# Kernel tuning notes

Measured on AMD Instinct MI355X. Metric: run time of the kernel, lower is better.

## Reference

```python
import jax, jax.numpy as jnp
import numpy as np

B, S, H, NH = 16, 384, 1024, 16
HD = H // NH  # head_dim = 64

def setup_inputs() -> dict:
    key = jax.random.key(0)
    k1, k2, k3 = jax.random.split(key, 3)
    activation = jax.random.normal(k1, (B, S, H), dtype=jnp.float32)
    attention_mask = jnp.zeros((B, 1, 1, S), dtype=jnp.float32)  # additive mask
    qkv_weight = jax.random.normal(k2, (H, 3 * H), dtype=jnp.float32) * 0.02
    qkv_bias = jax.random.normal(k3, (3 * H,), dtype=jnp.float32) * 0.02
    return {"activation": activation, "attention_mask": attention_mask,
            "qkv_weight": qkv_weight, "qkv_bias": qkv_bias}

def reference(activation, attention_mask, qkv_weight, qkv_bias):
    # op1: fused QKV projection
    qkv = activation @ qkv_weight + qkv_bias            # [B,S,3H]
    q, k, v = jnp.split(qkv, 3, axis=-1)                # each [B,S,H]
    # op2-6: split heads -> [B,NH,S,HD]
    def heads(x):
        return x.reshape(B, S, NH, HD).transpose(0, 2, 1, 3)
    q, k, v = heads(q), heads(k), heads(v)
    # op7: QK^T
    scores = jnp.einsum('bhqd,bhkd->bhqk', q, k)        # [B,NH,S,S]
    # op8: scale + mask + softmax (scale applied to scores, then additive mask)
    scale = 1.0 / np.sqrt(HD).astype(np.float32)
    probs = jax.nn.softmax(scores * scale + attention_mask, axis=-1)
    # op9: weighted V
    out = jnp.einsum('bhqk,bhkd->bhqd', probs, v)       # [B,NH,S,HD]
    # op10: concat heads
    return out.transpose(0, 2, 1, 3).reshape(B, S, H)
```

## Files before the change

### kernel.cpp

```cpp
#include <hip/hip_runtime.h>
#include <hip/hip_bf16.h>

#define BB 16
#define SS 384
#define HH 1024
#define NH 16
#define HD 64
#define MM (BB*SS)
#define KK HH
#define N3 (3*HH)

typedef float f32x4 __attribute__((ext_vector_type(4)));
typedef __bf16 bf16x8 __attribute__((ext_vector_type(8)));
typedef unsigned short us8 __attribute__((ext_vector_type(8)));
typedef unsigned short us4 __attribute__((ext_vector_type(4)));
typedef unsigned int u32x4 __attribute__((ext_vector_type(4)));

__device__ __forceinline__ void gload_lds16(const void* g, void* l) {
    __builtin_amdgcn_global_load_lds(
        (const __attribute__((address_space(1))) void*)g,
        (__attribute__((address_space(3))) void*)l, 16, 0, 0);
}

__device__ __forceinline__ unsigned short f2b(float f) {
    __bf16 h = (__bf16)f;
    return __builtin_bit_cast(unsigned short, h);
}

__global__ __launch_bounds__(256) void cvt_x(const float4* __restrict__ in,
                                             us4* __restrict__ out, int n4) {
    int i = blockIdx.x * 256 + threadIdx.x;
    if (i < n4) {
        float4 v = in[i];
        us4 o;
        o.x = f2b(v.x); o.y = f2b(v.y); o.z = f2b(v.z); o.w = f2b(v.w);
        out[i] = o;
    }
}

__global__ __launch_bounds__(256) void cvt_w(const float* __restrict__ Wf,
                                             __bf16* __restrict__ WT) {
    __shared__ float tile[32][33];
    const int n0 = blockIdx.x * 32, k0 = blockIdx.y * 32;
    const int t = threadIdx.x;
    const int tj = t & 31, ti = t >> 5;
#pragma unroll
    for (int p = 0; p < 4; ++p) {
        int i = p * 8 + ti;
        tile[i][tj] = Wf[(size_t)(k0 + i) * N3 + n0 + tj];
    }
    __syncthreads();
#pragma unroll
    for (int p = 0; p < 4; ++p) {
        int jj = p * 8 + ti;
        WT[(size_t)(n0 + jj) * KK + k0 + tj] = (__bf16)tile[tj][jj];
    }
}

__global__ __launch_bounds__(256) void qkv_gemm(const __bf16* __restrict__ Xb,
                                                const __bf16* __restrict__ WT,
                                                const float* __restrict__ bias,
                                                __bf16* __restrict__ QKb,
                                                __bf16* __restrict__ VTg) {
    __shared__ __bf16 As[128 * 32];
    __shared__ __bf16 Bs[128 * 32];
    const int t = threadIdx.x;
    const int w = t >> 6, lane = t & 63;
    const int wr = w >> 1, wc = w & 1;
    const int l15 = lane & 15, lg = lane >> 4;
    const int m0 = blockIdx.y * 128, n0 = blockIdx.x * 128;

    f32x4 acc[4][4] = {};

    for (int k0 = 0; k0 < KK; k0 += 32) {
#pragma unroll
        for (int i = 0; i < 2; ++i) {
            int slab = w * 2 + i;
            int row = slab * 16 + (lane >> 2);
            int ck = lane & 3;
            gload_lds16(Xb + (size_t)(m0 + row) * KK + k0 + ck * 8, &As[slab * 512]);
            gload_lds16(WT + (size_t)(n0 + row) * KK + k0 + ck * 8, &Bs[slab * 512]);
        }
        __syncthreads();

        bf16x8 a[4];
#pragma unroll
        for (int i = 0; i < 4; ++i) {
            int row = wr * 64 + i * 16 + l15;
            a[i] = *(const bf16x8*)&As[row * 32 + lg * 8];
        }
#pragma unroll
        for (int j = 0; j < 4; ++j) {
            int row = wc * 64 + j * 16 + l15;
            bf16x8 bv = *(const bf16x8*)&Bs[row * 32 + lg * 8];
#pragma unroll
            for (int i = 0; i < 4; ++i)
                acc[i][j] = __builtin_amdgcn_mfma_f32_16x16x32_bf16(a[i], bv, acc[i][j], 0, 0, 0);
        }
        __syncthreads();
    }

#pragma unroll
    for (int j = 0; j < 4; ++j) {
        int c = n0 + wc * 64 + j * 16 + l15;
        float bv = bias[c];
#pragma unroll
        for (int i = 0; i < 4; ++i) {
#pragma unroll
            for (int r = 0; r < 4; ++r) {
                int rr = m0 + wr * 64 + i * 16 + lg * 4 + r;
                float v = acc[i][j][r] + bv;
                if (c < 2048) {
                    QKb[(size_t)rr * 2048 + c] = (__bf16)v;
                } else {
                    int d = c & 63;
                    int hh = (c - 2048) >> 6;
                    int bb = rr / SS;
                    int s = rr - bb * SS;
                    VTg[((size_t)(bb * NH + hh) * HD + d) * SS + s] = (__bf16)v;
                }
            }
        }
    }
}

#define AKLOFF 0
#define AVTOFF 49152
#define AMKOFF 98304
#define ASMEM  99840

__global__ __launch_bounds__(512) void attn(const __bf16* __restrict__ QKb,
                                            const __bf16* __restrict__ VTg,
                                            const float* __restrict__ maskg,
                                            float* __restrict__ out) {
    extern __shared__ char smem[];
    const int head = blockIdx.x;
    const int b = head >> 4, h = head & 15;
    const int t = threadIdx.x;
    const int wv = t >> 6, lane = t & 63;
    const int l15 = lane & 15, lg = lane >> 4;

    bf16x8 bq[3][2];
#pragma unroll
    for (int c = 0; c < 3; ++c) {
        const size_t qr = (size_t)(b * SS + (wv + 8 * c) * 16 + l15) * 2048 + h * 64;
#pragma unroll
        for (int st = 0; st < 2; ++st)
            bq[c][st] = *(const bf16x8*)&QKb[qr + st * 32 + lg * 8];
    }

    for (int it = 0; it < 6; ++it) {
        int slot = it * 512 + t;
        int row = slot >> 3, ck = slot & 7;
        us8 v = *(const us8*)&QKb[(size_t)(b * SS + row) * 2048 + 1024 + h * 64 + ck * 8];
        int byte = (row * 128 + ck * 16) ^ ((row & 7) << 4);
        *(us8*)(smem + AKLOFF + byte) = v;
    }
    for (int it = 0; it < 6; ++it) {
        int slot = it * 512 + t;
        int d = slot / 48, ck = slot - d * 48;
        us8 v = *(const us8*)&VTg[((size_t)head * HD + d) * SS + ck * 8];
        int byte = (d * 768 + ck * 16) ^ ((d & 7) << 4);
        *(us8*)(smem + AVTOFF + byte) = v;
    }
    if (t < SS) ((float*)(smem + AMKOFF))[t] = maskg[b * SS + t];
    __syncthreads();

    const int srcA = l15 + 32 * (lg & 1);
    const int srcB = srcA + 16;
    const float* mrow = (const float*)(smem + AMKOFF);

#pragma unroll
    for (int c = 0; c < 3; ++c) {
        const int q0c = (wv + 8 * c) * 16;

        f32x4 acc[24];
#pragma unroll
        for (int f = 0; f < 24; ++f) acc[f] = f32x4{0.f, 0.f, 0.f, 0.f};
#pragma unroll
        for (int f = 0; f < 24; ++f) {
            int row = f * 16 + l15;
#pragma unroll
            for (int st = 0; st < 2; ++st) {
                bf16x8 kb = *(const bf16x8*)(smem + AKLOFF +
                             ((row * 128 + st * 64 + lg * 16) ^ ((row & 7) << 4)));
                acc[f] = __builtin_amdgcn_mfma_f32_16x16x32_bf16(kb, bq[c][st], acc[f], 0, 0, 0);
            }
        }

        float mx = -1e30f;
#pragma unroll
        for (int f = 0; f < 24; ++f) {
            float4 mk = *(const float4*)(mrow + f * 16 + 4 * lg);
            acc[f][0] = acc[f][0] * 0.125f + mk.x;
            acc[f][1] = acc[f][1] * 0.125f + mk.y;
            acc[f][2] = acc[f][2] * 0.125f + mk.z;
            acc[f][3] = acc[f][3] * 0.125f + mk.w;
            mx = fmaxf(mx, fmaxf(fmaxf(acc[f][0], acc[f][1]), fmaxf(acc[f][2], acc[f][3])));
        }
        mx = fmaxf(mx, __shfl_xor(mx, 16, 64));
        mx = fmaxf(mx, __shfl_xor(mx, 32, 64));

        float sm = 0.f;
#pragma unroll
        for (int f = 0; f < 24; ++f) {
#pragma unroll
            for (int r = 0; r < 4; ++r) {
                float p = __expf(acc[f][r] - mx);
                acc[f][r] = p;
                sm += p;
            }
        }
        sm += __shfl_xor(sm, 16, 64);
        sm += __shfl_xor(sm, 32, 64);
        const float inv = 1.f / sm;

        unsigned pk0[24], pk1[24];
#pragma unroll
        for (int f = 0; f < 24; ++f) {
            pk0[f] = (unsigned)f2b(acc[f][0]) | ((unsigned)f2b(acc[f][1]) << 16);
            pk1[f] = (unsigned)f2b(acc[f][2]) | ((unsigned)f2b(acc[f][3]) << 16);
        }

        u32x4 paw[12];
#pragma unroll
        for (int f = 0; f < 24; ++f) {
            unsigned a0 = __shfl(pk0[f], srcA, 64);
            unsigned a1 = __shfl(pk1[f], srcA, 64);
            unsigned b0 = __shfl(pk0[f], srcB, 64);
            unsigned b1 = __shfl(pk1[f], srcB, 64);
            if ((lg >> 1) == (f & 1))
                paw[f >> 1] = u32x4{a0, a1, b0, b1};
        }

        f32x4 o[4] = {};
#pragma unroll
        for (int st = 0; st < 12; ++st) {
            bf16x8 pa = __builtin_bit_cast(bf16x8, paw[st]);
#pragma unroll
            for (int j = 0; j < 4; ++j) {
                int d = j * 16 + l15;
                bf16x8 vb = *(const bf16x8*)(smem + AVTOFF +
                             ((d * 768 + st * 64 + lg * 16) ^ ((d & 7) << 4)));
                o[j] = __builtin_amdgcn_mfma_f32_16x16x32_bf16(pa, vb, o[j], 0, 0, 0);
            }
        }

#pragma unroll
        for (int r = 0; r < 4; ++r) {
            float invr = __shfl(inv, 4 * lg + r, 64);
            int qr = q0c + 4 * lg + r;
#pragma unroll
            for (int j = 0; j < 4; ++j)
                out[(size_t)(b * SS + qr) * HH + h * 64 + j * 16 + l15] =
                    o[j][r] * invr;
        }
    }
}

extern "C" void kernel_launch(void* const* d_in, const int* in_sizes, int n_in,
                              void* d_out, int out_size, void* d_ws, size_t ws_size,
                              hipStream_t stream) {
    const float* act  = (const float*)d_in[0];
    const float* mask = (const float*)d_in[1];
    const float* wq   = (const float*)d_in[2];
    const float* bias = (const float*)d_in[3];

    char* ws = (char*)d_ws;
    __bf16* Xb  = (__bf16*)(ws);
    __bf16* WT  = (__bf16*)(ws + 12582912);
    __bf16* QKb = (__bf16*)(ws + 18874368);
    __bf16* VTg = (__bf16*)(ws + 44040192);

    cvt_x<<<(MM * KK / 4 + 255) / 256, 256, 0, stream>>>((const float4*)act, (us4*)Xb, MM * KK / 4);
    cvt_w<<<dim3(N3 / 32, KK / 32), 256, 0, stream>>>(wq, WT);
    qkv_gemm<<<dim3(N3 / 128, MM / 128), 256, 0, stream>>>(Xb, WT, bias, QKb, VTg);

    (void)hipFuncSetAttribute((const void*)attn, hipFuncAttributeMaxDynamicSharedMemorySize, ASMEM);
    attn<<<BB * NH, 512, ASMEM, stream>>>(QKb, VTg, mask, (float*)d_out);
}
```

Measured before the change: 136.0 us.

## Split attention blocks by query half and stream V from global memory

The attention kernel now launches two 256-thread blocks per head, each covering half of the query rows, which doubles the grid from 256 to 512 blocks. V^T is no longer staged in LDS. It is read from global memory with a four-deep register prefetch that overlaps the PV MFMAs, and this halves LDS usage so more blocks can be resident per CU. Wave priority is raised around the MFMA loops. In exchange, each head's K tile is loaded twice, once per block, and V is read from global or cache per wave.

```diff
diff --git a/kernel.cpp b/kernel.cpp
--- a/kernel.cpp
+++ b/kernel.cpp
@@ -125,45 +125,54 @@
 }
 
 #define AKLOFF 0
-#define AVTOFF 49152
-#define AMKOFF 98304
-#define ASMEM  99840
-
-__global__ __launch_bounds__(512) void attn(const __bf16* __restrict__ QKb,
+#define AMKOFF 49152
+#define ASMEM  50688
+
+#define LOADV(VR, ST) do {                                                    \
+    _Pragma("unroll")                                                         \
+    for (int j = 0; j < 4; ++j)                                               \
+        VR[j] = *(const bf16x8*)&Vh[(size_t)(j * 16 + l15) * SS + (ST) * 32 + lg * 8]; \
+} while (0)
+
+#define PVST(VR, ST, NST) do {                                                \
+    bf16x8 pa = __builtin_bit_cast(bf16x8, paw[ST]);                          \
+    _Pragma("unroll")                                                         \
+    for (int j = 0; j < 4; ++j)                                               \
+        o[j] = __builtin_amdgcn_mfma_f32_16x16x32_bf16(pa, VR[j], o[j], 0, 0, 0); \
+    if ((NST) < 12) LOADV(VR, NST);                                           \
+} while (0)
+
+__global__ __launch_bounds__(256) void attn(const __bf16* __restrict__ QKb,
                                             const __bf16* __restrict__ VTg,
                                             const float* __restrict__ maskg,
                                             float* __restrict__ out) {
     extern __shared__ char smem[];
-    const int head = blockIdx.x;
+    const int bid = blockIdx.x;
+    const int head = bid >> 1, qh = bid & 1;
     const int b = head >> 4, h = head & 15;
     const int t = threadIdx.x;
     const int wv = t >> 6, lane = t & 63;
     const int l15 = lane & 15, lg = lane >> 4;
+    const __bf16* Vh = VTg + (size_t)head * HD * SS;
 
     bf16x8 bq[3][2];
 #pragma unroll
     for (int c = 0; c < 3; ++c) {
-        const size_t qr = (size_t)(b * SS + (wv + 8 * c) * 16 + l15) * 2048 + h * 64;
+        const size_t qr = (size_t)(b * SS + qh * 192 + (wv + 4 * c) * 16 + l15) * 2048 + h * 64;
 #pragma unroll
         for (int st = 0; st < 2; ++st)
             bq[c][st] = *(const bf16x8*)&QKb[qr + st * 32 + lg * 8];
     }
 
-    for (int it = 0; it < 6; ++it) {
-        int slot = it * 512 + t;
+    for (int it = 0; it < 12; ++it) {
+        int slot = it * 256 + t;
         int row = slot >> 3, ck = slot & 7;
         us8 v = *(const us8*)&QKb[(size_t)(b * SS + row) * 2048 + 1024 + h * 64 + ck * 8];
         int byte = (row * 128 + ck * 16) ^ ((row & 7) << 4);
         *(us8*)(smem + AKLOFF + byte) = v;
     }
-    for (int it = 0; it < 6; ++it) {
-        int slot = it * 512 + t;
-        int d = slot / 48, ck = slot - d * 48;
-        us8 v = *(const us8*)&VTg[((size_t)head * HD + d) * SS + ck * 8];
-        int byte = (d * 768 + ck * 16) ^ ((d & 7) << 4);
-        *(us8*)(smem + AVTOFF + byte) = v;
-    }
-    if (t < SS) ((float*)(smem + AMKOFF))[t] = maskg[b * SS + t];
+    for (int s = t; s < SS; s += 256)
+        ((float*)(smem + AMKOFF))[s] = maskg[b * SS + s];
     __syncthreads();
 
     const int srcA = l15 + 32 * (lg & 1);
@@ -172,11 +181,12 @@
 
 #pragma unroll
     for (int c = 0; c < 3; ++c) {
-        const int q0c = (wv + 8 * c) * 16;
+        const int q0c = qh * 192 + (wv + 4 * c) * 16;
 
         f32x4 acc[24];
 #pragma unroll
         for (int f = 0; f < 24; ++f) acc[f] = f32x4{0.f, 0.f, 0.f, 0.f};
+        __builtin_amdgcn_s_setprio(1);
 #pragma unroll
         for (int f = 0; f < 24; ++f) {
             int row = f * 16 + l15;
@@ -187,6 +197,10 @@
                 acc[f] = __builtin_amdgcn_mfma_f32_16x16x32_bf16(kb, bq[c][st], acc[f], 0, 0, 0);
             }
         }
+        __builtin_amdgcn_s_setprio(0);
+
+        bf16x8 va[4], vb_[4], vc[4], vd[4];
+        LOADV(va, 0); LOADV(vb_, 1); LOADV(vc, 2); LOADV(vd, 3);
 
         float mx = -1e30f;
 #pragma unroll
@@ -234,17 +248,11 @@
         }
 
         f32x4 o[4] = {};
-#pragma unroll
-        for (int st = 0; st < 12; ++st) {
-            bf16x8 pa = __builtin_bit_cast(bf16x8, paw[st]);
-#pragma unroll
-            for (int j = 0; j < 4; ++j) {
-                int d = j * 16 + l15;
-                bf16x8 vb = *(const bf16x8*)(smem + AVTOFF +
-                             ((d * 768 + st * 64 + lg * 16) ^ ((d & 7) << 4)));
-                o[j] = __builtin_amdgcn_mfma_f32_16x16x32_bf16(pa, vb, o[j], 0, 0, 0);
-            }
-        }
+        __builtin_amdgcn_s_setprio(1);
+        PVST(va, 0, 4);  PVST(vb_, 1, 5);  PVST(vc, 2, 6);   PVST(vd, 3, 7);
+        PVST(va, 4, 8);  PVST(vb_, 5, 9);  PVST(vc, 6, 10);  PVST(vd, 7, 11);
+        PVST(va, 8, 12); PVST(vb_, 9, 12); PVST(vc, 10, 12); PVST(vd, 11, 12);
+        __builtin_amdgcn_s_setprio(0);
 
 #pragma unroll
         for (int r = 0; r < 4; ++r) {
@@ -277,5 +285,5 @@
     qkv_gemm<<<dim3(N3 / 128, MM / 128), 256, 0, stream>>>(Xb, WT, bias, QKb, VTg);
 
     (void)hipFuncSetAttribute((const void*)attn, hipFuncAttributeMaxDynamicSharedMemorySize, ASMEM);
-    attn<<<BB * NH, 512, ASMEM, stream>>>(QKb, VTg, mask, (float*)d_out);
-}
+    attn<<<BB * NH * 2, 256, ASMEM, stream>>>(QKb, VTg, mask, (float*)d_out);
+}
```

Result: slower. 139.6 us (+2.6%).
